# Kernel optimization log

Hardware: AMD Instinct MI355X
Metric: run time of the kernel (lower is better)

Reference implementation:

```python
import jax, jax.numpy as jnp
import numpy as np

N = 10000
E = 160000
IN_CH, HID, OUT = 14, 128, 4
HEADS = 8
NEG_SLOPE = 0.2


def setup_inputs() -> dict:
    key = jax.random.key(0)
    ks = jax.random.split(key, 16)
    glorot = lambda k, shape: jax.random.normal(k, shape, jnp.float32) * np.sqrt(2.0 / (shape[0] + shape[-1]))
    inp = {
        'x': jax.random.normal(ks[0], (N, IN_CH), jnp.float32),
        'edge_index': jax.random.randint(ks[1], (2, E), 0, N, jnp.int64),
        # layer 1: 14 -> 8 heads x 128, concat
        'W1': glorot(ks[2], (IN_CH, HEADS * HID)),
        'a_src1': glorot(ks[3], (HEADS, HID)),
        'a_dst1': glorot(ks[4], (HEADS, HID)),
        'b1': jnp.zeros((HEADS * HID,), jnp.float32),
        # layer 2: 1024 -> 8 heads x 128, concat
        'W2': glorot(ks[5], (HEADS * HID, HEADS * HID)),
        'a_src2': glorot(ks[6], (HEADS, HID)),
        'a_dst2': glorot(ks[7], (HEADS, HID)),
        'b2': jnp.zeros((HEADS * HID,), jnp.float32),
        # layer 3: 1024 -> 1 head x 4, mean (concat=False)
        'W3': glorot(ks[8], (HEADS * HID, OUT)),
        'a_src3': glorot(ks[9], (1, OUT)),
        'a_dst3': glorot(ks[10], (1, OUT)),
        'b3': jnp.zeros((OUT,), jnp.float32),
    }
    return inp


def gat_conv(x, src, dst, W, a_src, a_dst, b, heads, out_ch, concat):
    n = x.shape[0]
    h = (x @ W).reshape(n, heads, out_ch)                      # [N,H,C]
    al_s = jnp.sum(h * a_src, axis=-1)                         # [N,H]
    al_d = jnp.sum(h * a_dst, axis=-1)                         # [N,H]
    e = al_s[src] + al_d[dst]                                  # [E,H]
    e = jnp.where(e > 0, e, NEG_SLOPE * e)                     # LeakyReLU(0.2)
    # segment softmax over incoming edges of each dst node
    m = jax.ops.segment_max(e, dst, num_segments=n)
    ex = jnp.exp(e - m[dst])
    z = jax.ops.segment_sum(ex, dst, num_segments=n)
    alpha = ex / (z[dst] + 1e-16)                              # [E,H]
    out = jax.ops.segment_sum(h[src] * alpha[:, :, None], dst, num_segments=n)  # [N,H,C]
    out = out.reshape(n, heads * out_ch) if concat else out.mean(axis=1)
    return out + b


def reference(x, edge_index, W1, a_src1, a_dst1, b1, W2, a_src2, a_dst2, b2, W3, a_src3, a_dst3, b3):
    n = x.shape[0]
    # add self-loops (PyG GATConv default)
    loop = jnp.arange(n, dtype=edge_index.dtype)
    src = jnp.concatenate([edge_index[0], loop])
    dst = jnp.concatenate([edge_index[1], loop])
    # dropout layers are identity in eval mode
    h = gat_conv(x, src, dst, W1, a_src1, a_dst1, b1, HEADS, HID, True)
    h = jax.nn.relu(h)
    h = gat_conv(h, src, dst, W2, a_src2, a_dst2, b2, HEADS, HID, True)
    h = jax.nn.relu(h)
    h = gat_conv(h, src, dst, W3, a_src3, a_dst3, b3, 1, OUT, False)
    h = jax.nn.relu(h)
    return h
```

## Files before the change

### kernel.cpp

```cpp
#include <hip/hip_runtime.h>

typedef unsigned short ushort_t;
typedef unsigned int uint32;

#define N_NODES 10000
#define N_EDGES 160000
#define ET (N_NODES + N_EDGES)
#define MPAD 10112
#define HT 1024
#define HEADS 8
#define NEG 0.2f
#define LOG2E 1.44269504088896f
#define EXP2(x) __builtin_amdgcn_exp2f(x)

#define O_FLAG     0
#define O_SRC      256
#define O_DST      (O_SRC + 680192)
#define O_COUNTS   (O_DST + 680192)
#define O_OFFS     (O_COUNTS + 40192)
#define O_CURS     (O_OFFS + 40192)
#define O_SSORT    (O_CURS + 40192)
#define O_ALS      (O_SSORT + 680192)
#define O_ALD      (O_ALS + 320000)
#define O_AL3S     (O_ALD + 320000)
#define O_AL3D     (O_AL3S + 40192)
#define O_H3       (O_AL3D + 40192)
#define O_XF       (O_H3 + 160000)
#define O_W1F      (O_XF + 560128)
#define O_AS1F     (O_W1F + 57344)
#define O_W3F      (O_AS1F + 24576)
#define O_S3F      (O_W3F + 16384)
#define O_W2T      (O_S3F + 768)
#define O_BUFA     (O_W2T + 2097152)
#define O_BUFB     (O_BUFA + 20709376)

__device__ __forceinline__ float bf2f(ushort_t u){ return __uint_as_float(((uint32)u) << 16); }
__device__ __forceinline__ ushort_t f2bf(float f){
    uint32 x = __float_as_uint(f);
    return (ushort_t)((x + 0x7fffu + ((x >> 16) & 1u)) >> 16);
}
__device__ __forceinline__ void unpack2(uint32 u, float& lo, float& hi){
    lo = __uint_as_float(u << 16);
    hi = __uint_as_float(u & 0xffff0000u);
}

typedef __bf16 bf16x8 __attribute__((ext_vector_type(8)));
typedef float  f32x4  __attribute__((ext_vector_type(4)));
typedef float  f32x2  __attribute__((ext_vector_type(2)));

__device__ __forceinline__ f32x2 unpk2(uint32 u){
    f32x2 r;
    r.x = __uint_as_float(u << 16);
    r.y = __uint_as_float(u & 0xffff0000u);
    return r;
}
__device__ __forceinline__ f32x2 pkfma(f32x2 a, f32x2 b, f32x2 c){
#if __has_builtin(__builtin_elementwise_fma)
    return __builtin_elementwise_fma(a, b, c);
#else
    f32x2 r; r.x = fmaf(a.x, b.x, c.x); r.y = fmaf(a.y, b.y, c.y); return r;
#endif
}

typedef const __attribute__((address_space(1))) uint32* gas1_u32;
typedef       __attribute__((address_space(3))) uint32* las3_u32;

__device__ __forceinline__ void gload_lds16(const void* g, void* l){
    __builtin_amdgcn_global_load_lds((gas1_u32)g, (las3_u32)l, 16, 0, 0);
}

__device__ __forceinline__ int probe_f32(const uint32* __restrict__ w){
    int cnt = 0;
    for (int i = 0; i < 256; i++){
        uint32 e = (w[i] >> 7) & 0xffu;
        cnt += (e >= 64u && e <= 160u) ? 1 : 0;
    }
    return (cnt > 200) ? 0 : 1;
}
__device__ __forceinline__ int probe_edge64(const int* __restrict__ ei){
    int nz = 0;
    for (int i = 0; i < 128; i++) nz |= ei[2*i + 1];
    return (nz == 0) ? 1 : 0;
}

__global__ __launch_bounds__(64) void k_probe(const uint32* __restrict__ w1raw,
                                              const int* __restrict__ eiraw,
                                              int* __restrict__ flags){
    if (threadIdx.x == 0) flags[1] = probe_f32(w1raw);
    if (threadIdx.x == 1) flags[0] = probe_edge64(eiraw);
}

struct CvtArgs {
    const void* src[12];
    float*      dst[12];
    int         n[12];
    float       scl[12];
};

__global__ __launch_bounds__(256) void k_setup(CvtArgs a, const void* __restrict__ W2,
                                               int* __restrict__ counts,
                                               ushort_t* __restrict__ W2T,
                                               const int* __restrict__ flags){
    __shared__ ushort_t tile[32][33];
    int slice = blockIdx.y;
    int tid = threadIdx.x;
    if (slice < 12){
        int n = a.n[slice];
        int base = blockIdx.x * 1024 + tid * 4;
        if (base >= n) return;
        int f32 = flags[1];
        float scl = a.scl[slice];
        const void* s = a.src[slice];
        float* d = a.dst[slice];
        #pragma unroll
        for (int j = 0; j < 4; j++){
            int i = base + j;
            if (i < n) d[i] = scl * (f32 ? ((const float*)s)[i] : bf2f(((const ushort_t*)s)[i]));
        }
    } else if (slice == 12){
        if (blockIdx.x < 10){
            int i0 = blockIdx.x * 1024 + tid * 4;
            if (i0 + 3 < N_NODES){
                *(int4*)(counts + i0) = make_int4(0,0,0,0);
            } else {
                for (int j = 0; j < 4; j++) if (i0 + j < N_NODES) counts[i0 + j] = 0;
            }
        }
    } else {
        int f32 = flags[1];
        int bx = blockIdx.x & 31, by = blockIdx.x >> 5;
        int cx = tid & 31;
        int ry = (tid >> 5) * 4;
        #pragma unroll
        for (int r = 0; r < 4; r++){
            size_t idx = (size_t)(by*32 + ry + r)*1024 + bx*32 + cx;
            tile[ry + r][cx] = f32 ? f2bf(((const float*)W2)[idx]) : ((const ushort_t*)W2)[idx];
        }
        __syncthreads();
        #pragma unroll
        for (int r = 0; r < 4; r++)
            W2T[(size_t)(bx*32 + ry + r)*1024 + by*32 + cx] = tile[cx][ry + r];
    }
}

__global__ __launch_bounds__(256) void k_extract_hist(const void* __restrict__ ei, const int* __restrict__ flags,
                                                      int* __restrict__ src, int* __restrict__ dst,
                                                      int* __restrict__ counts){
    int i = blockIdx.x * 256 + threadIdx.x;
    int is64 = flags[0];
    int s = -1, d = -1;
    if (i < N_EDGES){
        if (is64){
            const long long* p = (const long long*)ei;
            s = (int)p[i]; d = (int)p[N_EDGES + i];
        } else {
            const int* p = (const int*)ei;
            s = p[i]; d = p[N_EDGES + i];
        }
    } else if (i < ET){
        s = i - N_EDGES; d = s;
    }
    if (d >= 0){
        src[i] = s; dst[i] = d;
        atomicAdd(&counts[d], 1);
    }
}

__global__ __launch_bounds__(1024) void k_scan(const int* __restrict__ counts, int* __restrict__ offs,
                                               int* __restrict__ cursors, int n){
    __shared__ int wsum[16];
    int tid = threadIdx.x;
    int lane = tid & 63, wid = tid >> 6;
    int base = tid * 10;
    int pfx[10];
    int s = 0;
    #pragma unroll
    for (int j = 0; j < 10; j++){
        int i = base + j;
        pfx[j] = s;
        int c = (i < n) ? counts[i] : 0;
        s += c;
    }
    int x = s;
    #pragma unroll
    for (int d = 1; d < 64; d <<= 1){
        int t = __shfl_up(x, d, 64);
        if (lane >= d) x += t;
    }
    if (lane == 63) wsum[wid] = x;
    __syncthreads();
    if (wid == 0 && lane < 16){
        int w = wsum[lane];
        #pragma unroll
        for (int d = 1; d < 16; d <<= 1){
            int t = __shfl_up(w, d, 64);
            if (lane >= d) w += t;
        }
        wsum[lane] = w;
    }
    __syncthreads();
    int wprefix = (wid == 0) ? 0 : wsum[wid - 1];
    int excl = wprefix + (x - s);
    #pragma unroll
    for (int j = 0; j < 10; j++){
        int i = base + j;
        if (i < n){ offs[i] = excl + pfx[j]; cursors[i] = excl + pfx[j]; }
    }
    if (tid == 1023) offs[n] = wprefix + x;
}

__global__ __launch_bounds__(256) void k_scatter(const int* __restrict__ src, const int* __restrict__ dst,
                                                 int* __restrict__ cursors, int* __restrict__ ssort){
    int i = blockIdx.x * 256 + threadIdx.x;
    if (i < ET){
        int pos = atomicAdd(&cursors[dst[i]], 1);
        ssort[pos] = src[i] * 8;
    }
}

__global__ __launch_bounds__(256) void k_gemm1f(const float* __restrict__ x, const float* __restrict__ W1,
                                                const float* __restrict__ a_src, const float* __restrict__ a_dst,
                                                ushort_t* __restrict__ h1,
                                                float* __restrict__ alS, float* __restrict__ alD){
    int tid = threadIdx.x;
    int c0 = tid * 4;
    float4 w1r[14];
    #pragma unroll
    for (int k = 0; k < 14; k++) w1r[k] = *(const float4*)(W1 + k*HT + c0);
    float4 sv = *(const float4*)(a_src + c0);
    float4 dv = *(const float4*)(a_dst + c0);
    int head = tid >> 5, l32 = tid & 31;
    for (int n = blockIdx.x; n < N_NODES; n += gridDim.x){
        float a0=0.f, a1=0.f, a2=0.f, a3=0.f;
        #pragma unroll
        for (int k = 0; k < 14; k++){
            float xv = x[n*14 + k];
            float4 w = w1r[k];
            a0 += xv*w.x; a1 += xv*w.y; a2 += xv*w.z; a3 += xv*w.w;
        }
        uint2 o;
        o.x = (uint32)f2bf(a0) | ((uint32)f2bf(a1) << 16);
        o.y = (uint32)f2bf(a2) | ((uint32)f2bf(a3) << 16);
        *(uint2*)(h1 + (size_t)n*HT + c0) = o;
        float h0,h1v,h2,h3v;
        unpack2(o.x, h0, h1v); unpack2(o.y, h2, h3v);
        float s = h0*sv.x + h1v*sv.y + h2*sv.z + h3v*sv.w;
        float d = h0*dv.x + h1v*dv.y + h2*dv.z + h3v*dv.w;
        #pragma unroll
        for (int of = 16; of; of >>= 1){ s += __shfl_xor(s, of, 32); d += __shfl_xor(d, of, 32); }
        if (l32 == 0){ alS[n*HEADS + head] = s; alD[n*HEADS + head] = d; }
    }
}

__global__ __launch_bounds__(256) void k_gat_agg(const ushort_t* __restrict__ H, const float* __restrict__ alS,
                                                 const float* __restrict__ alD, const int* __restrict__ offs,
                                                 const int* __restrict__ srcs, const float* __restrict__ bias,
                                                 ushort_t* __restrict__ out){
    int tid = threadIdx.x;
    int wv = tid >> 6, lane = tid & 63;
    int head = blockIdx.x & 7;
    int n = (blockIdx.x >> 3) * 4 + wv;
    if (n >= N_NODES) return;
    int beg = offs[n], end = offs[n+1];
    int g = lane >> 4;
    int q = lane & 15;
    float ad = alD[n*HEADS + head];
    const ushort_t* Hh = H + head*128 + q*8;
    const float NINF = -__int_as_float(0x7f800000);

    float m = -1e30f, z = 0.f;
    f32x2 C0 = (f32x2)0.f, C1 = (f32x2)0.f, C2 = (f32x2)0.f, C3 = (f32x2)0.f;
    for (int c = beg; c < end; c += 64){
        int cn = min(64, end - c);
        int sreg = (lane < cn) ? srcs[c + lane] : 0;
        int j = 0;
        for (; j + 16 <= cn; j += 16){
            int s0 = __shfl(sreg, j + g, 64);
            int s1 = __shfl(sreg, j + 4 + g, 64);
            int s2 = __shfl(sreg, j + 8 + g, 64);
            int s3 = __shfl(sreg, j + 12 + g, 64);
            uint4 u0 = *(const uint4*)(Hh + (size_t)s0*128);
            uint4 u1 = *(const uint4*)(Hh + (size_t)s1*128);
            uint4 u2 = *(const uint4*)(Hh + (size_t)s2*128);
            uint4 u3 = *(const uint4*)(Hh + (size_t)s3*128);
            float v0 = alS[s0 + head] + ad; v0 = v0 > 0.f ? v0 : NEG*v0;
            float v1 = alS[s1 + head] + ad; v1 = v1 > 0.f ? v1 : NEG*v1;
            float v2 = alS[s2 + head] + ad; v2 = v2 > 0.f ? v2 : NEG*v2;
            float v3 = alS[s3 + head] + ad; v3 = v3 > 0.f ? v3 : NEG*v3;
            float vm = fmaxf(fmaxf(v0, v1), fmaxf(v2, v3));
            if (vm > m){
                f32x2 scv = (f32x2)EXP2(m - vm);
                z *= scv.x;
                C0 *= scv; C1 *= scv; C2 *= scv; C3 *= scv;
                m = vm;
            }
            float w0 = EXP2(v0 - m);
            float w1 = EXP2(v1 - m);
            float w2 = EXP2(v2 - m);
            float w3 = EXP2(v3 - m);
            z += (w0 + w1) + (w2 + w3);
            f32x2 w0v = (f32x2)w0, w1v = (f32x2)w1, w2v = (f32x2)w2, w3v = (f32x2)w3;
            C0 = pkfma(w0v, unpk2(u0.x), pkfma(w1v, unpk2(u1.x), C0));
            C1 = pkfma(w0v, unpk2(u0.y), pkfma(w1v, unpk2(u1.y), C1));
            C2 = pkfma(w0v, unpk2(u0.z), pkfma(w1v, unpk2(u1.z), C2));
            C3 = pkfma(w0v, unpk2(u0.w), pkfma(w1v, unpk2(u1.w), C3));
            C0 = pkfma(w2v, unpk2(u2.x), pkfma(w3v, unpk2(u3.x), C0));
            C1 = pkfma(w2v, unpk2(u2.y), pkfma(w3v, unpk2(u3.y), C1));
            C2 = pkfma(w2v, unpk2(u2.z), pkfma(w3v, unpk2(u3.z), C2));
            C3 = pkfma(w2v, unpk2(u2.w), pkfma(w3v, unpk2(u3.w), C3));
        }
        for (; j + 8 <= cn; j += 8){
            int s0 = __shfl(sreg, j + g, 64);
            int s1 = __shfl(sreg, j + 4 + g, 64);
            uint4 u0 = *(const uint4*)(Hh + (size_t)s0*128);
            uint4 u1 = *(const uint4*)(Hh + (size_t)s1*128);
            float v0 = alS[s0 + head] + ad; v0 = v0 > 0.f ? v0 : NEG*v0;
            float v1 = alS[s1 + head] + ad; v1 = v1 > 0.f ? v1 : NEG*v1;
            float vm = fmaxf(v0, v1);
            if (vm > m){
                f32x2 scv = (f32x2)EXP2(m - vm);
                z *= scv.x;
                C0 *= scv; C1 *= scv; C2 *= scv; C3 *= scv;
                m = vm;
            }
            float w0 = EXP2(v0 - m);
            float w1 = EXP2(v1 - m);
            z += (w0 + w1);
            f32x2 w0v = (f32x2)w0, w1v = (f32x2)w1;
            C0 = pkfma(w0v, unpk2(u0.x), pkfma(w1v, unpk2(u1.x), C0));
            C1 = pkfma(w0v, unpk2(u0.y), pkfma(w1v, unpk2(u1.y), C1));
            C2 = pkfma(w0v, unpk2(u0.z), pkfma(w1v, unpk2(u1.z), C2));
            C3 = pkfma(w0v, unpk2(u0.w), pkfma(w1v, unpk2(u1.w), C3));
        }
        for (; j < cn; j += 4){
            int e = j + g;
            int s0 = __shfl(sreg, e, 64);
            uint4 u0 = *(const uint4*)(Hh + (size_t)s0*128);
            float v0 = alS[s0 + head] + ad; v0 = v0 > 0.f ? v0 : NEG*v0;
            v0 = (e < cn) ? v0 : NINF;
            if (v0 > m){
                f32x2 scv = (f32x2)EXP2(m - v0);
                z *= scv.x;
                C0 *= scv; C1 *= scv; C2 *= scv; C3 *= scv;
                m = v0;
            }
            float w0 = EXP2(v0 - m);
            z += w0;
            f32x2 w0v = (f32x2)w0;
            C0 = pkfma(w0v, unpk2(u0.x), C0);
            C1 = pkfma(w0v, unpk2(u0.y), C1);
            C2 = pkfma(w0v, unpk2(u0.z), C2);
            C3 = pkfma(w0v, unpk2(u0.w), C3);
        }
    }
    #pragma unroll
    for (int off = 16; off < 64; off <<= 1){
        float m2 = __shfl_xor(m, off, 64);
        float z2 = __shfl_xor(z, off, 64);
        f32x2 D0, D1, D2, D3;
        D0.x = __shfl_xor(C0.x, off, 64); D0.y = __shfl_xor(C0.y, off, 64);
        D1.x = __shfl_xor(C1.x, off, 64); D1.y = __shfl_xor(C1.y, off, 64);
        D2.x = __shfl_xor(C2.x, off, 64); D2.y = __shfl_xor(C2.y, off, 64);
        D3.x = __shfl_xor(C3.x, off, 64); D3.y = __shfl_xor(C3.y, off, 64);
        float nm = fmaxf(m, m2);
        float a = EXP2(m - nm), b = EXP2(m2 - nm);
        z = z*a + z2*b;
        f32x2 av = (f32x2)a, bv = (f32x2)b;
        C0 = C0*av + D0*bv; C1 = C1*av + D1*bv;
        C2 = C2*av + D2*bv; C3 = C3*av + D3*bv;
        m = nm;
    }
    if (g == 0){
        float inv = 1.f / (z + 1e-16f);
        int ch0 = head*128 + q*8;
        float4 b0 = *(const float4*)(bias + ch0);
        float4 b1 = *(const float4*)(bias + ch0 + 4);
        float c0 = fmaxf(C0.x*inv+b0.x, 0.f), c1 = fmaxf(C0.y*inv+b0.y, 0.f);
        float c2 = fmaxf(C1.x*inv+b0.z, 0.f), c3 = fmaxf(C1.y*inv+b0.w, 0.f);
        float c4 = fmaxf(C2.x*inv+b1.x, 0.f), c5 = fmaxf(C2.y*inv+b1.y, 0.f);
        float c6 = fmaxf(C3.x*inv+b1.z, 0.f), c7 = fmaxf(C3.y*inv+b1.w, 0.f);
        uint4 o;
        o.x = (uint32)f2bf(c0) | ((uint32)f2bf(c1) << 16);
        o.y = (uint32)f2bf(c2) | ((uint32)f2bf(c3) << 16);
        o.z = (uint32)f2bf(c4) | ((uint32)f2bf(c5) << 16);
        o.w = (uint32)f2bf(c6) | ((uint32)f2bf(c7) << 16);
        *(uint4*)(out + (size_t)n*HT + ch0) = o;
    }
}

__global__ __launch_bounds__(512) void k_gemm2(const ushort_t* __restrict__ A, const ushort_t* __restrict__ BT,
                                               ushort_t* __restrict__ C,
                                               const float* __restrict__ aS, const float* __restrict__ aD,
                                               float* __restrict__ alS, float* __restrict__ alD){
    __shared__ ushort_t lbuf[2][2][128*64];
    float (*reds)[3][64][2] = (float (*)[3][64][2])lbuf;
    int L = blockIdx.x;
    int xcd = L & 7;
    int wi  = L >> 3;
    int bm  = xcd * 10 + (wi >> 3);
    int bn  = wi & 7;
    if (bm >= 79) return;
    int tid = threadIdx.x;
    int lane = tid & 63;
    int wave = tid >> 6;
    int wm  = (wave & 1) * 64;
    int wn32 = (wave >> 1) * 32;
    int lm = lane & 15, kg = lane >> 4;
    int c0 = (kg ^ (lm & 7)) * 8;
    f32x4 acc[4][2];
    #pragma unroll
    for (int i = 0; i < 4; i++)
        #pragma unroll
        for (int j = 0; j < 2; j++) acc[i][j] = (f32x4)0.0f;

    const int K = 1024;
    int rowA0 = bm * 128, rowB0 = bn * 128;

    auto stage = [&](int buf, int k0){
        #pragma unroll
        for (int it = 0; it < 2; ++it){
            int s = tid + it*512;
            int r = s >> 3;
            int q = (s & 7) ^ (r & 7);
            gload_lds16(A  + (size_t)(rowA0 + r)*K + k0 + q*8, &lbuf[buf][0][s*8]);
            gload_lds16(BT + (size_t)(rowB0 + r)*K + k0 + q*8, &lbuf[buf][1][s*8]);
        }
    };

    stage(0, 0);
    asm volatile("s_waitcnt vmcnt(0)" ::: "memory");
    __syncthreads();
    int cur = 0;
    for (int k0 = 0; k0 < K; k0 += 64){
        if (k0 + 64 < K) stage(cur ^ 1, k0 + 64);
        bf16x8 a0[4], a1[4], b0[2], b1[2];
        #pragma unroll
        for (int mt = 0; mt < 4; mt++){
            const ushort_t* base = &lbuf[cur][0][(wm + mt*16 + lm)*64];
            a0[mt] = *(const bf16x8*)(base + c0);
            a1[mt] = *(const bf16x8*)(base + (c0 ^ 32));
        }
        #pragma unroll
        for (int nt = 0; nt < 2; nt++){
            const ushort_t* base = &lbuf[cur][1][(wn32 + nt*16 + lm)*64];
            b0[nt] = *(const bf16x8*)(base + c0);
            b1[nt] = *(const bf16x8*)(base + (c0 ^ 32));
        }
        #pragma unroll
        for (int mt = 0; mt < 4; mt++)
            #pragma unroll
            for (int nt = 0; nt < 2; nt++)
                acc[mt][nt] = __builtin_amdgcn_mfma_f32_16x16x32_bf16(a0[mt], b0[nt], acc[mt][nt], 0, 0, 0);
        #pragma unroll
        for (int mt = 0; mt < 4; mt++)
            #pragma unroll
            for (int nt = 0; nt < 2; nt++)
                acc[mt][nt] = __builtin_amdgcn_mfma_f32_16x16x32_bf16(a1[mt], b1[nt], acc[mt][nt], 0, 0, 0);
        asm volatile("s_waitcnt vmcnt(0)" ::: "memory");
        __syncthreads();
        cur ^= 1;
    }
    #pragma unroll
    for (int mt = 0; mt < 4; mt++){
        int row_base = bm*128 + wm + mt*16 + kg*4;
        #pragma unroll
        for (int nt = 0; nt < 2; nt++){
            int col = bn*128 + wn32 + nt*16 + lm;
            #pragma unroll
            for (int r = 0; r < 4; r++){
                int row = row_base + r;
                if (row < N_NODES) C[(size_t)row*HT + col] = f2bf(acc[mt][nt][r]);
            }
        }
    }
    float as_l[2], ad_l[2];
    #pragma unroll
    for (int nt = 0; nt < 2; nt++){
        as_l[nt] = aS[bn*128 + wn32 + nt*16 + lm];
        ad_l[nt] = aD[bn*128 + wn32 + nt*16 + lm];
    }
    float psA[4][4], pdA[4][4];
    #pragma unroll
    for (int mt = 0; mt < 4; mt++){
        #pragma unroll
        for (int r = 0; r < 4; r++){
            float ps = acc[mt][0][r]*as_l[0] + acc[mt][1][r]*as_l[1];
            float pd = acc[mt][0][r]*ad_l[0] + acc[mt][1][r]*ad_l[1];
            #pragma unroll
            for (int o = 1; o < 16; o <<= 1){ ps += __shfl_xor(ps, o, 64); pd += __shfl_xor(pd, o, 64); }
            psA[mt][r] = ps; pdA[mt][r] = pd;
            if (wn32 != 0 && lm == 0){
                int rl = mt*16 + kg*4 + r;
                reds[wm >> 6][(wn32 >> 5) - 1][rl][0] = ps;
                reds[wm >> 6][(wn32 >> 5) - 1][rl][1] = pd;
            }
        }
    }
    __syncthreads();
    if (wn32 == 0 && lm == 0){
        #pragma unroll
        for (int mt = 0; mt < 4; mt++){
            #pragma unroll
            for (int r = 0; r < 4; r++){
                int rl = mt*16 + kg*4 + r;
                int row = bm*128 + wm + rl;
                if (row < N_NODES){
                    alS[row*HEADS + bn] = psA[mt][r] + reds[wm >> 6][0][rl][0]
                                        + reds[wm >> 6][1][rl][0] + reds[wm >> 6][2][rl][0];
                    alD[row*HEADS + bn] = pdA[mt][r] + reds[wm >> 6][0][rl][1]
                                        + reds[wm >> 6][1][rl][1] + reds[wm >> 6][2][rl][1];
                }
            }
        }
    }
}

__global__ __launch_bounds__(256) void k_gemm3(const ushort_t* __restrict__ A, const float* __restrict__ W3,
                                               const float* __restrict__ s3,
                                               float* __restrict__ h3, float* __restrict__ al3s, float* __restrict__ al3d){
    int tid = threadIdx.x;
    int lane = tid & 63, wave = tid >> 6;
    int n = blockIdx.x * 4 + wave;
    if (n >= N_NODES) return;
    float4 w3r[16];
    #pragma unroll
    for (int j = 0; j < 16; j++) w3r[j] = ((const float4*)W3)[lane*16 + j];
    const uint4* ap = (const uint4*)(A + (size_t)n*HT + lane*16);
    uint4 u0 = ap[0], u1 = ap[1];
    uint32 uu[8] = {u0.x,u0.y,u0.z,u0.w,u1.x,u1.y,u1.z,u1.w};
    float acc0=0.f, acc1=0.f, acc2=0.f, acc3=0.f;
    #pragma unroll
    for (int p = 0; p < 8; p++){
        float lo, hi;
        unpack2(uu[p], lo, hi);
        float4 wl = w3r[p*2], wh = w3r[p*2+1];
        acc0 += lo*wl.x + hi*wh.x;
        acc1 += lo*wl.y + hi*wh.y;
        acc2 += lo*wl.z + hi*wh.z;
        acc3 += lo*wl.w + hi*wh.w;
    }
    #pragma unroll
    for (int o = 32; o; o >>= 1){
        acc0 += __shfl_xor(acc0, o, 64); acc1 += __shfl_xor(acc1, o, 64);
        acc2 += __shfl_xor(acc2, o, 64); acc3 += __shfl_xor(acc3, o, 64);
    }
    if (lane == 0){
        *(float4*)(h3 + n*4) = make_float4(acc0, acc1, acc2, acc3);
        al3s[n] = acc0*s3[0] + acc1*s3[1] + acc2*s3[2] + acc3*s3[3];
        al3d[n] = acc0*s3[16] + acc1*s3[17] + acc2*s3[18] + acc3*s3[19];
    }
}

__global__ __launch_bounds__(256) void k_gat_agg3(const float* __restrict__ h3, const float* __restrict__ al3s,
                                                  const float* __restrict__ al3d, const int* __restrict__ offs,
                                                  const int* __restrict__ srcs, const float* __restrict__ b3,
                                                  const int* __restrict__ flags, void* __restrict__ out){
    int tid = threadIdx.x;
    int l = tid & 63, wave = tid >> 6;
    int n = blockIdx.x * 4 + wave;
    if (n >= N_NODES) return;
    int beg = offs[n], end = offs[n+1];
    float ad = al3d[n];
    float m = -1e30f;
    for (int e = beg + l; e < end; e += 64){
        float v = al3s[srcs[e] >> 3] + ad; v = v > 0.f ? v : NEG*v;
        m = fmaxf(m, v);
    }
    #pragma unroll
    for (int o = 32; o; o >>= 1) m = fmaxf(m, __shfl_xor(m, o, 64));
    float z = 0.f;
    for (int e = beg + l; e < end; e += 64){
        float v = al3s[srcs[e] >> 3] + ad; v = v > 0.f ? v : NEG*v;
        z += EXP2(v - m);
    }
    #pragma unroll
    for (int o = 32; o; o >>= 1) z += __shfl_xor(z, o, 64);
    float inv = 1.f / (z + 1e-16f);
    float a0=0.f, a1=0.f, a2=0.f, a3=0.f;
    for (int e = beg + l; e < end; e += 64){
        int sp = srcs[e];
        float v = al3s[sp >> 3] + ad; v = v > 0.f ? v : NEG*v;
        float w = EXP2(v - m) * inv;
        float4 hv = *(const float4*)(h3 + (sp >> 1));
        a0 += w*hv.x; a1 += w*hv.y; a2 += w*hv.z; a3 += w*hv.w;
    }
    #pragma unroll
    for (int o = 32; o; o >>= 1){
        a0 += __shfl_xor(a0, o, 64); a1 += __shfl_xor(a1, o, 64);
        a2 += __shfl_xor(a2, o, 64); a3 += __shfl_xor(a3, o, 64);
    }
    if (l == 0){
        float r0 = fmaxf(a0 + b3[0], 0.f);
        float r1 = fmaxf(a1 + b3[1], 0.f);
        float r2 = fmaxf(a2 + b3[2], 0.f);
        float r3 = fmaxf(a3 + b3[3], 0.f);
        if (flags[1]){
            float* o4 = (float*)out;
            o4[n*4+0]=r0; o4[n*4+1]=r1; o4[n*4+2]=r2; o4[n*4+3]=r3;
        } else {
            ushort_t* o2 = (ushort_t*)out;
            o2[n*4+0]=f2bf(r0); o2[n*4+1]=f2bf(r1); o2[n*4+2]=f2bf(r2); o2[n*4+3]=f2bf(r3);
        }
    }
}

extern "C" void kernel_launch(void* const* d_in, const int* in_sizes, int n_in,
                              void* d_out, int out_size, void* d_ws, size_t ws_size,
                              hipStream_t stream){
    const void* x   = d_in[0];
    const void* ei  = d_in[1];
    const void* W1  = d_in[2];
    const void* as1 = d_in[3];
    const void* ad1 = d_in[4];
    const void* b1  = d_in[5];
    const void* W2  = d_in[6];
    const void* as2 = d_in[7];
    const void* ad2 = d_in[8];
    const void* b2  = d_in[9];
    const void* W3  = d_in[10];
    const void* as3 = d_in[11];
    const void* ad3 = d_in[12];
    const void* b3  = d_in[13];

    char* ws = (char*)d_ws;
    int* flags     = (int*)(ws + O_FLAG);
    int* srcA      = (int*)(ws + O_SRC);
    int* dstA      = (int*)(ws + O_DST);
    int* counts    = (int*)(ws + O_COUNTS);
    int* offs      = (int*)(ws + O_OFFS);
    int* cursors   = (int*)(ws + O_CURS);
    int* ssort     = (int*)(ws + O_SSORT);
    float* alS     = (float*)(ws + O_ALS);
    float* alD     = (float*)(ws + O_ALD);
    float* al3s    = (float*)(ws + O_AL3S);
    float* al3d    = (float*)(ws + O_AL3D);
    float* h3      = (float*)(ws + O_H3);
    float* xF      = (float*)(ws + O_XF);
    float* W1F     = (float*)(ws + O_W1F);
    float* wvecF   = (float*)(ws + O_AS1F);
    float* W3F     = (float*)(ws + O_W3F);
    float* s3F     = (float*)(ws + O_S3F);
    ushort_t* W2T  = (ushort_t*)(ws + O_W2T);
    ushort_t* bufA = (ushort_t*)(ws + O_BUFA);
    ushort_t* bufB = (ushort_t*)(ws + O_BUFB);

    const int EB = (ET + 255) / 256;

    CvtArgs ca;
    ca.src[0]=x;   ca.dst[0]=xF;            ca.n[0]=140000;  ca.scl[0]=1.0f;
    ca.src[1]=W1;  ca.dst[1]=W1F;           ca.n[1]=14336;   ca.scl[1]=1.0f;
    ca.src[2]=as1; ca.dst[2]=wvecF+0*1024;  ca.n[2]=1024;    ca.scl[2]=LOG2E;
    ca.src[3]=ad1; ca.dst[3]=wvecF+1*1024;  ca.n[3]=1024;    ca.scl[3]=LOG2E;
    ca.src[4]=b1;  ca.dst[4]=wvecF+2*1024;  ca.n[4]=1024;    ca.scl[4]=1.0f;
    ca.src[5]=as2; ca.dst[5]=wvecF+3*1024;  ca.n[5]=1024;    ca.scl[5]=LOG2E;
    ca.src[6]=ad2; ca.dst[6]=wvecF+4*1024;  ca.n[6]=1024;    ca.scl[6]=LOG2E;
    ca.src[7]=b2;  ca.dst[7]=wvecF+5*1024;  ca.n[7]=1024;    ca.scl[7]=1.0f;
    ca.src[8]=W3;  ca.dst[8]=W3F;           ca.n[8]=4096;    ca.scl[8]=1.0f;
    ca.src[9]=as3; ca.dst[9]=s3F+0;         ca.n[9]=4;       ca.scl[9]=LOG2E;
    ca.src[10]=ad3; ca.dst[10]=s3F+16;      ca.n[10]=4;      ca.scl[10]=LOG2E;
    ca.src[11]=b3;  ca.dst[11]=s3F+32;      ca.n[11]=4;      ca.scl[11]=1.0f;

    k_probe<<<1, 64, 0, stream>>>((const uint32*)W1, (const int*)ei, flags);
    k_setup<<<dim3(1024, 14), 256, 0, stream>>>(ca, W2, counts, W2T, flags);
    k_extract_hist<<<EB, 256, 0, stream>>>(ei, flags, srcA, dstA, counts);
    k_scan<<<1, 1024, 0, stream>>>(counts, offs, cursors, N_NODES);
    k_scatter<<<EB, 256, 0, stream>>>(srcA, dstA, cursors, ssort);

    k_gemm1f<<<512, 256, 0, stream>>>(xF, W1F, wvecF+0*1024, wvecF+1*1024, bufA, alS, alD);
    k_gat_agg<<<20000, 256, 0, stream>>>(bufA, alS, alD, offs, ssort, wvecF+2*1024, bufB);

    k_gemm2<<<640, 512, 0, stream>>>(bufB, W2T, bufA, wvecF+3*1024, wvecF+4*1024, alS, alD);
    k_gat_agg<<<20000, 256, 0, stream>>>(bufA, alS, alD, offs, ssort, wvecF+5*1024, bufB);

    k_gemm3<<<2500, 256, 0, stream>>>(bufB, W3F, s3F, h3, al3s, al3d);
    k_gat_agg3<<<2500, 256, 0, stream>>>(h3, al3s, al3d, offs, ssort, s3F+32, flags, d_out);
}
```

Before: 306.4 us.

## Pipeline gemm2 K-loop with four 32-wide LDS stages and partial vmcnt waits

Restructures the layer-2 GEMM main loop from double-buffered 64-wide K tiles with full vmcnt(0) drains into a four-buffer, 32-wide K pipeline that prefetches three tiles ahead. It waits only on the oldest loads using vmcnt(4) and raw s_barrier. An XOR swizzle adapted to 32-element rows keeps LDS reads conflict-free. The goal is to hide global-load latency behind MFMA work, at the cost of twice as many barriers and smaller compute per iteration.

```diff
diff --git a/kernel.cpp b/kernel.cpp
--- a/kernel.cpp
+++ b/kernel.cpp
@@ -392,7 +392,7 @@
                                                ushort_t* __restrict__ C,
                                                const float* __restrict__ aS, const float* __restrict__ aD,
                                                float* __restrict__ alS, float* __restrict__ alD){
-    __shared__ ushort_t lbuf[2][2][128*64];
+    __shared__ ushort_t lbuf[4][2][128*32];
     float (*reds)[3][64][2] = (float (*)[3][64][2])lbuf;
     int L = blockIdx.x;
     int xcd = L & 7;
@@ -406,7 +406,8 @@
     int wm  = (wave & 1) * 64;
     int wn32 = (wave >> 1) * 32;
     int lm = lane & 15, kg = lane >> 4;
-    int c0 = (kg ^ (lm & 7)) * 8;
+    int sw = (lm & 3) ^ ((lm >> 2) & 3);
+    int cq = (kg ^ sw) * 8;
     f32x4 acc[4][2];
     #pragma unroll
     for (int i = 0; i < 4; i++)
@@ -414,52 +415,51 @@
         for (int j = 0; j < 2; j++) acc[i][j] = (f32x4)0.0f;
 
     const int K = 1024;
+    const int NT = 32;
     int rowA0 = bm * 128, rowB0 = bn * 128;
 
-    auto stage = [&](int buf, int k0){
-        #pragma unroll
-        for (int it = 0; it < 2; ++it){
-            int s = tid + it*512;
-            int r = s >> 3;
-            int q = (s & 7) ^ (r & 7);
-            gload_lds16(A  + (size_t)(rowA0 + r)*K + k0 + q*8, &lbuf[buf][0][s*8]);
-            gload_lds16(BT + (size_t)(rowB0 + r)*K + k0 + q*8, &lbuf[buf][1][s*8]);
-        }
+    auto stage = [&](int t){
+        int buf = t & 3;
+        int k0 = t * 32;
+        int s = tid;
+        int r = s >> 2;
+        int q = (s & 3) ^ ((r & 3) ^ ((r >> 2) & 3));
+        gload_lds16(A  + (size_t)(rowA0 + r)*K + k0 + q*8, &lbuf[buf][0][s*8]);
+        gload_lds16(BT + (size_t)(rowB0 + r)*K + k0 + q*8, &lbuf[buf][1][s*8]);
     };
-
-    stage(0, 0);
-    asm volatile("s_waitcnt vmcnt(0)" ::: "memory");
-    __syncthreads();
-    int cur = 0;
-    for (int k0 = 0; k0 < K; k0 += 64){
-        if (k0 + 64 < K) stage(cur ^ 1, k0 + 64);
-        bf16x8 a0[4], a1[4], b0[2], b1[2];
-        #pragma unroll
-        for (int mt = 0; mt < 4; mt++){
-            const ushort_t* base = &lbuf[cur][0][(wm + mt*16 + lm)*64];
-            a0[mt] = *(const bf16x8*)(base + c0);
-            a1[mt] = *(const bf16x8*)(base + (c0 ^ 32));
-        }
-        #pragma unroll
-        for (int nt = 0; nt < 2; nt++){
-            const ushort_t* base = &lbuf[cur][1][(wn32 + nt*16 + lm)*64];
-            b0[nt] = *(const bf16x8*)(base + c0);
-            b1[nt] = *(const bf16x8*)(base + (c0 ^ 32));
-        }
+    auto compute = [&](int t){
+        int buf = t & 3;
+        bf16x8 a[4], b[2];
+        #pragma unroll
+        for (int mt = 0; mt < 4; mt++)
+            a[mt] = *(const bf16x8*)(&lbuf[buf][0][(wm + mt*16 + lm)*32 + cq]);
+        #pragma unroll
+        for (int nt = 0; nt < 2; nt++)
+            b[nt] = *(const bf16x8*)(&lbuf[buf][1][(wn32 + nt*16 + lm)*32 + cq]);
         #pragma unroll
         for (int mt = 0; mt < 4; mt++)
             #pragma unroll
             for (int nt = 0; nt < 2; nt++)
-                acc[mt][nt] = __builtin_amdgcn_mfma_f32_16x16x32_bf16(a0[mt], b0[nt], acc[mt][nt], 0, 0, 0);
-        #pragma unroll
-        for (int mt = 0; mt < 4; mt++)
-            #pragma unroll
-            for (int nt = 0; nt < 2; nt++)
-                acc[mt][nt] = __builtin_amdgcn_mfma_f32_16x16x32_bf16(a1[mt], b1[nt], acc[mt][nt], 0, 0, 0);
-        asm volatile("s_waitcnt vmcnt(0)" ::: "memory");
-        __syncthreads();
-        cur ^= 1;
-    }
+                acc[mt][nt] = __builtin_amdgcn_mfma_f32_16x16x32_bf16(a[mt], b[nt], acc[mt][nt], 0, 0, 0);
+    };
+
+    stage(0); stage(1); stage(2);
+    for (int t = 0; t < NT - 2; ++t){
+        asm volatile("s_waitcnt vmcnt(4)" ::: "memory");
+        __builtin_amdgcn_s_barrier();
+        if (t + 3 < NT) stage(t + 3);
+        compute(t);
+        asm volatile("s_waitcnt lgkmcnt(0)" ::: "memory");
+    }
+    asm volatile("s_waitcnt vmcnt(2)" ::: "memory");
+    __builtin_amdgcn_s_barrier();
+    compute(NT - 2);
+    asm volatile("s_waitcnt lgkmcnt(0)" ::: "memory");
+    asm volatile("s_waitcnt vmcnt(0)" ::: "memory");
+    __builtin_amdgcn_s_barrier();
+    compute(NT - 1);
+    __syncthreads();
+
     #pragma unroll
     for (int mt = 0; mt < 4; mt++){
         int row_base = bm*128 + wm + mt*16 + kg*4;
```

Measured after the change: 307.6 us (median of 2 runs). No clear change (+0.4%).
